# Optimization experiments

Measured on AMD Instinct MI355X. Metric: run time of the kernel, lower is better.

Reference implementation:

```python
import jax, jax.numpy as jnp
import numpy as np

B, C, H, W = 8, 256, 64, 64
CK = 64  # C // k with k=4


def setup_inputs() -> dict:
    key = jax.random.key(0)
    ks = jax.random.split(key, 5)
    s = 1.0 / np.sqrt(C)
    return {
        "x": jax.random.normal(ks[0], (B, C, H, W), dtype=jnp.float32),
        "wq": jax.random.normal(ks[1], (CK, C), dtype=jnp.float32) * s,
        "bq": jnp.zeros((CK,), dtype=jnp.float32),
        "wk": jax.random.normal(ks[2], (CK, C), dtype=jnp.float32) * s,
        "bk": jnp.zeros((CK,), dtype=jnp.float32),
        "wv": jax.random.normal(ks[3], (C, C), dtype=jnp.float32) * s,
        "bv": jnp.zeros((C,), dtype=jnp.float32),
        "wg": jax.random.normal(ks[4], (C, C), dtype=jnp.float32) * s,
        "bg": jnp.zeros((C,), dtype=jnp.float32),
    }


def reference(x, wq, bq, wk, bk, wv, bv, wg, bg):
    b, c, h, w = x.shape
    n = h * w
    xf = x.reshape(b, c, n)  # [B, C, N]
    # 1x1 convs are channel-wise matmuls
    q = jnp.einsum('oc,bcn->bon', wq, xf) + bq[None, :, None]  # [B, Ck, N]
    k = jnp.einsum('oc,bcn->bon', wk, xf) + bk[None, :, None]  # [B, Ck, N]
    v = jnp.einsum('oc,bcn->bon', wv, xf) + bv[None, :, None]  # [B, C, N]
    # energy[b,i,j] = q[b,:,i] . k[b,:,j]
    energy = jnp.einsum('bci,bcj->bij', q, k)  # [B, N, N]
    energy = jax.nn.elu(energy) / n
    out = jnp.einsum('bcn,bnj->bcj', v, energy).reshape(b, c, h, w)
    out = jnp.einsum('oc,bchw->bohw', wg, out) + bg[None, :, None, None]
    return out
```

## Files before the change

### kernel.cpp

```cpp
#include <hip/hip_runtime.h>
#include <math.h>

#define BATCH 8
#define CH    256
#define NPIX  4096
#define CKDIM 64

typedef __attribute__((ext_vector_type(8))) short short8;
typedef __attribute__((ext_vector_type(4))) float f32x4;

#define MFMA16x16(a, b, c) __builtin_amdgcn_mfma_f32_16x16x32_bf16((a), (b), (c), 0, 0, 0)

__device__ __forceinline__ unsigned short f2bf(float f) {
    union { float f; unsigned int u; } v; v.f = f;
    unsigned int u = v.u;
    u += 0x7fffu + ((u >> 16) & 1u);
    return (unsigned short)(u >> 16);
}

__global__ void prep_kernel(const float* __restrict__ wq, const float* __restrict__ bq,
                            const float* __restrict__ wk, const float* __restrict__ bk,
                            const float* __restrict__ wv, const float* __restrict__ bv,
                            const float* __restrict__ wg,
                            unsigned short* __restrict__ W_all, float* __restrict__ bias_all) {
    int o = blockIdx.x;
    int c = threadIdx.x;
    if (o < 64) {
        W_all[o * CH + c] = f2bf(wq[o * CH + c]);
        if (c == 0) bias_all[o] = bq[o];
    } else if (o < 128) {
        int oo = o - 64;
        W_all[o * CH + c] = f2bf(wk[oo * CH + c]);
        if (c == 0) bias_all[o] = bk[oo];
    } else {
        int oo = o - 128;
        float acc = 0.f;
        for (int m = 0; m < CH; ++m)
            acc += wg[oo * CH + m] * wv[m * CH + c];
        W_all[o * CH + c] = f2bf(acc);
        if (c == 0) {
            float b = 0.f;
            for (int m = 0; m < CH; ++m) b += wg[oo * CH + m] * bv[m];
            bias_all[o] = b;
        }
    }
}

__global__ void xpose_kernel(const float* __restrict__ x, unsigned short* __restrict__ xt) {
    __shared__ float Tl[64][65];
    int n0 = blockIdx.x * 64;
    int c0 = blockIdx.y * 64;
    int b  = blockIdx.z;
    int tid = threadIdx.x;

#pragma unroll
    for (int r = 0; r < 4; ++r) {
        int f  = r * 256 + tid;
        int c  = f >> 4;
        int n4 = f & 15;
        float4 v = *(const float4*)(x + ((size_t)b * CH + c0 + c) * NPIX + n0 + n4 * 4);
        Tl[n4 * 4 + 0][c] = v.x;
        Tl[n4 * 4 + 1][c] = v.y;
        Tl[n4 * 4 + 2][c] = v.z;
        Tl[n4 * 4 + 3][c] = v.w;
    }
    __syncthreads();
#pragma unroll
    for (int r = 0; r < 2; ++r) {
        int f    = r * 256 + tid;
        int nrow = f >> 3;
        int c8   = f & 7;
        unsigned int pk[4];
#pragma unroll
        for (int p = 0; p < 4; ++p) {
            unsigned int lo = f2bf(Tl[nrow][c8 * 8 + p * 2 + 0]);
            unsigned int hi = f2bf(Tl[nrow][c8 * 8 + p * 2 + 1]);
            pk[p] = lo | (hi << 16);
        }
        *(uint4*)(xt + ((size_t)b * NPIX + n0 + nrow) * CH + c0 + c8 * 8) = *(uint4*)pk;
    }
}

__global__ void qkv_mfma(const unsigned short* __restrict__ xt,
                         const unsigned short* __restrict__ W_all,
                         const float* __restrict__ bias_all,
                         unsigned short* __restrict__ qk, unsigned short* __restrict__ vp) {
    __shared__ __align__(16) unsigned short Xl[64][264];

    int n0   = blockIdx.x * 64;
    int b    = blockIdx.y;
    int tid  = threadIdx.x;
    int lane = tid & 63;
    int w    = tid >> 6;
    int col  = lane & 15;
    int quad = lane >> 4;

#pragma unroll
    for (int r = 0; r < 8; ++r) {
        int f   = r * 256 + tid;
        int row = f >> 5;
        int c8  = f & 31;
        *(uint4*)&Xl[row][c8 * 8] = *(const uint4*)(xt + ((size_t)b * NPIX + n0 + row) * CH + c8 * 8);
    }
    __syncthreads();

#pragma unroll
    for (int og = 0; og < 6; ++og) {
        int o0 = og * 64;
        const unsigned short* Arow = W_all + (size_t)(o0 + w * 16 + col) * CH + quad * 8;

        f32x4 acc[4];
#pragma unroll
        for (int t = 0; t < 4; ++t) acc[t] = (f32x4){0.f, 0.f, 0.f, 0.f};

#pragma unroll
        for (int kc = 0; kc < 8; ++kc) {
            short8 a = *(const short8*)(Arow + kc * 32);
#pragma unroll
            for (int nt = 0; nt < 4; ++nt) {
                short8 bb = *(const short8*)&Xl[nt * 16 + col][kc * 32 + quad * 8];
                acc[nt] = MFMA16x16(a, bb, acc[nt]);
            }
        }

        float4 bias = *(const float4*)(bias_all + o0 + w * 16 + quad * 4);
        float bs[4] = {bias.x, bias.y, bias.z, bias.w};

        if (og < 2) {
#pragma unroll
            for (int nt = 0; nt < 4; ++nt) {
                int n = n0 + nt * 16 + col;
                unsigned int pk[2];
#pragma unroll
                for (int p = 0; p < 2; ++p) {
                    unsigned int lo = f2bf(acc[nt][p * 2 + 0] + bs[p * 2 + 0]);
                    unsigned int hi = f2bf(acc[nt][p * 2 + 1] + bs[p * 2 + 1]);
                    pk[p] = lo | (hi << 16);
                }
                *(uint2*)(qk + ((size_t)b * NPIX + n) * 128 + o0 + w * 16 + quad * 4) = *(uint2*)pk;
            }
        } else {
#pragma unroll
            for (int nt = 0; nt < 4; ++nt) {
                int n = n0 + nt * 16 + col;
#pragma unroll
                for (int r = 0; r < 4; ++r) {
                    int oo = o0 - 128 + w * 16 + quad * 4 + r;
                    vp[((size_t)b * CH + oo) * NPIX + n] = f2bf(acc[nt][r] + bs[r]);
                }
            }
        }
    }
}

#define LPK 72
__global__ __launch_bounds__(512, 4)
void attn_v4(const unsigned short* __restrict__ qk,
             const unsigned short* __restrict__ vp,
             const float* __restrict__ bg, float* __restrict__ out) {
    __shared__ __align__(16) unsigned short Qt[64][LPK];
    __shared__ __align__(16) unsigned short Vl[256][LPK];
    __shared__ __align__(16) unsigned short St[64][LPK];

    int j0   = blockIdx.x * 64;
    int b    = blockIdx.y;
    int tid  = threadIdx.x;
    int lane = tid & 63;
    int w    = tid >> 6;
    int col  = lane & 15;
    int quad = lane >> 4;

    int tjA = w & 3;
    int tiP = (w >> 2) * 2;

    short8 bK[2];
#pragma unroll
    for (int ks = 0; ks < 2; ++ks)
        bK[ks] = *(const short8*)(qk + ((size_t)b * NPIX + j0 + tjA * 16 + col) * 128 + 64 + ks * 32 + quad * 8);

    f32x4 acc[2][4];
#pragma unroll
    for (int ot = 0; ot < 2; ++ot)
#pragma unroll
        for (int tj = 0; tj < 4; ++tj) acc[ot][tj] = (f32x4){0.f, 0.f, 0.f, 0.f};

    for (int i0 = 0; i0 < NPIX; i0 += 64) {
        __syncthreads();

        {
            int row = tid >> 3, q8 = tid & 7;
            *(uint4*)&Qt[row][q8 * 8] =
                *(const uint4*)(qk + ((size_t)b * NPIX + i0 + row) * 128 + q8 * 8);
        }
#pragma unroll
        for (int r = 0; r < 4; ++r) {
            int f = r * 512 + tid;
            int row = f >> 3, q8 = f & 7;
            *(uint4*)&Vl[row][q8 * 8] =
                *(const uint4*)(vp + ((size_t)b * CH + row) * NPIX + i0 + q8 * 8);
        }
        __syncthreads();

#pragma unroll
        for (int t = 0; t < 2; ++t) {
            int ti = tiP + t;
            short8 a0 = *(const short8*)&Qt[ti * 16 + col][quad * 8];
            short8 a1 = *(const short8*)&Qt[ti * 16 + col][32 + quad * 8];
            f32x4 s = (f32x4){0.f, 0.f, 0.f, 0.f};
            s = MFMA16x16(a0, bK[0], s);
            s = MFMA16x16(a1, bK[1], s);
            unsigned int pk[2];
#pragma unroll
            for (int p = 0; p < 2; ++p) {
                float e0 = s[p * 2 + 0];
                float e1 = s[p * 2 + 1];
                e0 = (e0 > 0.f) ? e0 : (__expf(e0) - 1.f);
                e1 = (e1 > 0.f) ? e1 : (__expf(e1) - 1.f);
                e0 *= (1.f / (float)NPIX);
                e1 *= (1.f / (float)NPIX);
                pk[p] = (unsigned int)f2bf(e0) | ((unsigned int)f2bf(e1) << 16);
            }
            *(uint2*)&St[tjA * 16 + col][ti * 16 + quad * 4] = *(uint2*)pk;
        }
        __syncthreads();

#pragma unroll
        for (int ks = 0; ks < 2; ++ks) {
            short8 sb[4];
#pragma unroll
            for (int tj = 0; tj < 4; ++tj)
                sb[tj] = *(const short8*)&St[tj * 16 + col][ks * 32 + quad * 8];
#pragma unroll
            for (int ot = 0; ot < 2; ++ot) {
                short8 bv = *(const short8*)&Vl[(w * 2 + ot) * 16 + col][ks * 32 + quad * 8];
#pragma unroll
                for (int tj = 0; tj < 4; ++tj)
                    acc[ot][tj] = MFMA16x16(sb[tj], bv, acc[ot][tj]);
            }
        }
    }

#pragma unroll
    for (int ot = 0; ot < 2; ++ot) {
        int o = (w * 2 + ot) * 16 + col;
        float bgv = bg[o];
#pragma unroll
        for (int tj = 0; tj < 4; ++tj) {
            int j = j0 + tj * 16 + quad * 4;
            float4 st;
            st.x = acc[ot][tj][0] + bgv;
            st.y = acc[ot][tj][1] + bgv;
            st.z = acc[ot][tj][2] + bgv;
            st.w = acc[ot][tj][3] + bgv;
            *(float4*)&out[((size_t)b * CH + o) * NPIX + j] = st;
        }
    }
}

extern "C" void kernel_launch(void* const* d_in, const int* in_sizes, int n_in,
                              void* d_out, int out_size, void* d_ws, size_t ws_size,
                              hipStream_t stream) {
    const float* x  = (const float*)d_in[0];
    const float* wq = (const float*)d_in[1];
    const float* bq = (const float*)d_in[2];
    const float* wk = (const float*)d_in[3];
    const float* bk = (const float*)d_in[4];
    const float* wv = (const float*)d_in[5];
    const float* bv = (const float*)d_in[6];
    const float* wg = (const float*)d_in[7];
    const float* bg = (const float*)d_in[8];
    float* out = (float*)d_out;

    unsigned short* W_all = (unsigned short*)d_ws;
    float* bias_all = (float*)(W_all + 384 * 256);
    unsigned short* xt = (unsigned short*)(bias_all + 384);
    unsigned short* qk = xt + (size_t)BATCH * NPIX * CH;
    unsigned short* vp = qk + (size_t)BATCH * NPIX * 128;

    prep_kernel<<<dim3(384), dim3(256), 0, stream>>>(wq, bq, wk, bk, wv, bv, wg, W_all, bias_all);
    xpose_kernel<<<dim3(NPIX / 64, CH / 64, BATCH), dim3(256), 0, stream>>>(x, xt);
    qkv_mfma<<<dim3(NPIX / 64, BATCH), dim3(256), 0, stream>>>(xt, W_all, bias_all, qk, vp);
    attn_v4<<<dim3(NPIX / 64, BATCH), dim3(512), 0, stream>>>(qk, vp, bg, out);
}
```

Measured before the change: 267.8 us.

## Software-pipeline attention loop with double-buffered Q/S and register-resident V

The attention kernel now double-buffers the Q tile and score tile in shared memory. Scores for tile t are computed while the V-multiply runs on the scores of tile t-1, which cuts the loop to a single barrier per iteration. V fragments are loaded straight from global memory into registers instead of being staged in shared memory. Q and K are split into separate contiguous buffers, and the weight-prep kernel is reorganized to compute 8 output rows per block with wg cached in shared memory. The changes raise register pressure and add prefetch complexity.

```diff
diff --git a/kernel.cpp b/kernel.cpp
--- a/kernel.cpp
+++ b/kernel.cpp
@@ -23,25 +23,41 @@
                             const float* __restrict__ wv, const float* __restrict__ bv,
                             const float* __restrict__ wg,
                             unsigned short* __restrict__ W_all, float* __restrict__ bias_all) {
-    int o = blockIdx.x;
-    int c = threadIdx.x;
-    if (o < 64) {
-        W_all[o * CH + c] = f2bf(wq[o * CH + c]);
-        if (c == 0) bias_all[o] = bq[o];
-    } else if (o < 128) {
-        int oo = o - 64;
-        W_all[o * CH + c] = f2bf(wk[oo * CH + c]);
-        if (c == 0) bias_all[o] = bk[oo];
+    int bo  = blockIdx.x;
+    int tid = threadIdx.x;
+    if (bo < 16) {
+        int r0 = bo * 8;
+#pragma unroll
+        for (int r = 0; r < 8; ++r) {
+            int o = r0 + r;
+            float v = (o < 64) ? wq[o * CH + tid] : wk[(o - 64) * CH + tid];
+            W_all[o * CH + tid] = f2bf(v);
+        }
+        if (tid < 8) {
+            int o = r0 + tid;
+            bias_all[o] = (o < 64) ? bq[o] : bk[o - 64];
+        }
     } else {
-        int oo = o - 128;
-        float acc = 0.f;
-        for (int m = 0; m < CH; ++m)
-            acc += wg[oo * CH + m] * wv[m * CH + c];
-        W_all[o * CH + c] = f2bf(acc);
-        if (c == 0) {
-            float b = 0.f;
-            for (int m = 0; m < CH; ++m) b += wg[oo * CH + m] * bv[m];
-            bias_all[o] = b;
+        int ob = (bo - 16) * 8;
+        __shared__ float wgl[8][256];
+#pragma unroll
+        for (int r = 0; r < 8; ++r) wgl[r][tid] = wg[(size_t)(ob + r) * CH + tid];
+        __syncthreads();
+        float acc[8];
+#pragma unroll
+        for (int r = 0; r < 8; ++r) acc[r] = 0.f;
+        for (int m = 0; m < CH; ++m) {
+            float wvv = wv[(size_t)m * CH + tid];
+#pragma unroll
+            for (int r = 0; r < 8; ++r) acc[r] += wgl[r][m] * wvv;
+        }
+#pragma unroll
+        for (int r = 0; r < 8; ++r)
+            W_all[(size_t)(128 + ob + r) * CH + tid] = f2bf(acc[r]);
+        if (tid < 8) {
+            float bb = 0.f;
+            for (int m = 0; m < CH; ++m) bb += wgl[tid][m] * bv[m];
+            bias_all[128 + ob + tid] = bb;
         }
     }
 }
@@ -84,7 +100,8 @@
 __global__ void qkv_mfma(const unsigned short* __restrict__ xt,
                          const unsigned short* __restrict__ W_all,
                          const float* __restrict__ bias_all,
-                         unsigned short* __restrict__ qk, unsigned short* __restrict__ vp) {
+                         unsigned short* __restrict__ qg, unsigned short* __restrict__ kg,
+                         unsigned short* __restrict__ vp) {
     __shared__ __align__(16) unsigned short Xl[64][264];
 
     int n0   = blockIdx.x * 64;
@@ -127,6 +144,7 @@
         float bs[4] = {bias.x, bias.y, bias.z, bias.w};
 
         if (og < 2) {
+            unsigned short* dst = (og == 0) ? qg : kg;
 #pragma unroll
             for (int nt = 0; nt < 4; ++nt) {
                 int n = n0 + nt * 16 + col;
@@ -137,7 +155,7 @@
                     unsigned int hi = f2bf(acc[nt][p * 2 + 1] + bs[p * 2 + 1]);
                     pk[p] = lo | (hi << 16);
                 }
-                *(uint2*)(qk + ((size_t)b * NPIX + n) * 128 + o0 + w * 16 + quad * 4) = *(uint2*)pk;
+                *(uint2*)(dst + ((size_t)b * NPIX + n) * 64 + w * 16 + quad * 4) = *(uint2*)pk;
             }
         } else {
 #pragma unroll
@@ -153,14 +171,14 @@
     }
 }
 
-#define LPK 72
+#define LQ 72
 __global__ __launch_bounds__(512, 4)
-void attn_v4(const unsigned short* __restrict__ qk,
+void attn_v6(const unsigned short* __restrict__ qg,
+             const unsigned short* __restrict__ kg,
              const unsigned short* __restrict__ vp,
              const float* __restrict__ bg, float* __restrict__ out) {
-    __shared__ __align__(16) unsigned short Qt[64][LPK];
-    __shared__ __align__(16) unsigned short Vl[256][LPK];
-    __shared__ __align__(16) unsigned short St[64][LPK];
+    __shared__ __align__(16) unsigned short Qt[2][64][LQ];
+    __shared__ __align__(16) unsigned short St[2][64][LQ];
 
     int j0   = blockIdx.x * 64;
     int b    = blockIdx.y;
@@ -170,13 +188,20 @@
     int col  = lane & 15;
     int quad = lane >> 4;
 
-    int tjA = w & 3;
-    int tiP = (w >> 2) * 2;
-
-    short8 bK[2];
-#pragma unroll
-    for (int ks = 0; ks < 2; ++ks)
-        bK[ks] = *(const short8*)(qk + ((size_t)b * NPIX + j0 + tjA * 16 + col) * 128 + 64 + ks * 32 + quad * 8);
+    int tiw = w >> 1;
+    int tjh = w & 1;
+
+    const size_t nb = (size_t)b * NPIX;
+    int srow = tid >> 3, sq8 = tid & 7;
+
+    short8 bK[2][2];
+#pragma unroll
+    for (int tjl = 0; tjl < 2; ++tjl)
+#pragma unroll
+        for (int ks = 0; ks < 2; ++ks)
+            bK[tjl][ks] = *(const short8*)(kg + (nb + j0 + (tjh * 2 + tjl) * 16 + col) * 64 + ks * 32 + quad * 8);
+
+    *(uint4*)&Qt[0][srow][sq8 * 8] = *(const uint4*)(qg + (nb + srow) * 64 + sq8 * 8);
 
     f32x4 acc[2][4];
 #pragma unroll
@@ -184,60 +209,96 @@
 #pragma unroll
         for (int tj = 0; tj < 4; ++tj) acc[ot][tj] = (f32x4){0.f, 0.f, 0.f, 0.f};
 
-    for (int i0 = 0; i0 < NPIX; i0 += 64) {
-        __syncthreads();
-
-        {
-            int row = tid >> 3, q8 = tid & 7;
-            *(uint4*)&Qt[row][q8 * 8] =
-                *(const uint4*)(qk + ((size_t)b * NPIX + i0 + row) * 128 + q8 * 8);
-        }
-#pragma unroll
-        for (int r = 0; r < 4; ++r) {
-            int f = r * 512 + tid;
-            int row = f >> 3, q8 = f & 7;
-            *(uint4*)&Vl[row][q8 * 8] =
-                *(const uint4*)(vp + ((size_t)b * CH + row) * NPIX + i0 + q8 * 8);
-        }
-        __syncthreads();
-
-#pragma unroll
-        for (int t = 0; t < 2; ++t) {
-            int ti = tiP + t;
-            short8 a0 = *(const short8*)&Qt[ti * 16 + col][quad * 8];
-            short8 a1 = *(const short8*)&Qt[ti * 16 + col][32 + quad * 8];
+    __syncthreads();
+
+    uint4 qn = *(const uint4*)(qg + (nb + 64 + srow) * 64 + sq8 * 8);
+    {
+        short8 aq0 = *(const short8*)&Qt[0][tiw * 16 + col][quad * 8];
+        short8 aq1 = *(const short8*)&Qt[0][tiw * 16 + col][32 + quad * 8];
+#pragma unroll
+        for (int tjl = 0; tjl < 2; ++tjl) {
             f32x4 s = (f32x4){0.f, 0.f, 0.f, 0.f};
-            s = MFMA16x16(a0, bK[0], s);
-            s = MFMA16x16(a1, bK[1], s);
+            s = MFMA16x16(aq0, bK[tjl][0], s);
+            s = MFMA16x16(aq1, bK[tjl][1], s);
             unsigned int pk[2];
 #pragma unroll
             for (int p = 0; p < 2; ++p) {
-                float e0 = s[p * 2 + 0];
-                float e1 = s[p * 2 + 1];
+                float e0 = s[p * 2 + 0], e1 = s[p * 2 + 1];
                 e0 = (e0 > 0.f) ? e0 : (__expf(e0) - 1.f);
                 e1 = (e1 > 0.f) ? e1 : (__expf(e1) - 1.f);
                 e0 *= (1.f / (float)NPIX);
                 e1 *= (1.f / (float)NPIX);
                 pk[p] = (unsigned int)f2bf(e0) | ((unsigned int)f2bf(e1) << 16);
             }
-            *(uint2*)&St[tjA * 16 + col][ti * 16 + quad * 4] = *(uint2*)pk;
-        }
-        __syncthreads();
+            *(uint2*)&St[0][(tjh * 2 + tjl) * 16 + col][tiw * 16 + quad * 4] = *(uint2*)pk;
+        }
+    }
+    *(uint4*)&Qt[1][srow][sq8 * 8] = qn;
+    uint4 aV[2][2];
+#pragma unroll
+    for (int ot = 0; ot < 2; ++ot)
+#pragma unroll
+        for (int ks = 0; ks < 2; ++ks)
+            aV[ot][ks] = *(const uint4*)(vp + ((size_t)b * CH + (2 * w + ot) * 16 + col) * NPIX + ks * 32 + quad * 8);
+    __syncthreads();
+
+    for (int t = 1; t < 64; ++t) {
+        int i0 = t * 64;
+        int p  = t & 1;
+        uint4 q2 = *(const uint4*)(qg + (nb + (((t + 1) & 63) * 64) + srow) * 64 + sq8 * 8);
+
+        short8 aq0 = *(const short8*)&Qt[p][tiw * 16 + col][quad * 8];
+        short8 aq1 = *(const short8*)&Qt[p][tiw * 16 + col][32 + quad * 8];
+#pragma unroll
+        for (int tjl = 0; tjl < 2; ++tjl) {
+            f32x4 s = (f32x4){0.f, 0.f, 0.f, 0.f};
+            s = MFMA16x16(aq0, bK[tjl][0], s);
+            s = MFMA16x16(aq1, bK[tjl][1], s);
+            unsigned int pk[2];
+#pragma unroll
+            for (int pp = 0; pp < 2; ++pp) {
+                float e0 = s[pp * 2 + 0], e1 = s[pp * 2 + 1];
+                e0 = (e0 > 0.f) ? e0 : (__expf(e0) - 1.f);
+                e1 = (e1 > 0.f) ? e1 : (__expf(e1) - 1.f);
+                e0 *= (1.f / (float)NPIX);
+                e1 *= (1.f / (float)NPIX);
+                pk[pp] = (unsigned int)f2bf(e0) | ((unsigned int)f2bf(e1) << 16);
+            }
+            *(uint2*)&St[p][(tjh * 2 + tjl) * 16 + col][tiw * 16 + quad * 4] = *(uint2*)pk;
+        }
+        *(uint4*)&Qt[p ^ 1][srow][sq8 * 8] = q2;
 
 #pragma unroll
         for (int ks = 0; ks < 2; ++ks) {
             short8 sb[4];
 #pragma unroll
             for (int tj = 0; tj < 4; ++tj)
-                sb[tj] = *(const short8*)&St[tj * 16 + col][ks * 32 + quad * 8];
-#pragma unroll
-            for (int ot = 0; ot < 2; ++ot) {
-                short8 bv = *(const short8*)&Vl[(w * 2 + ot) * 16 + col][ks * 32 + quad * 8];
+                sb[tj] = *(const short8*)&St[p ^ 1][tj * 16 + col][ks * 32 + quad * 8];
+#pragma unroll
+            for (int ot = 0; ot < 2; ++ot)
 #pragma unroll
                 for (int tj = 0; tj < 4; ++tj)
-                    acc[ot][tj] = MFMA16x16(sb[tj], bv, acc[ot][tj]);
-            }
-        }
+                    acc[ot][tj] = MFMA16x16(sb[tj], *(const short8*)&aV[ot][ks], acc[ot][tj]);
+        }
+#pragma unroll
+        for (int ot = 0; ot < 2; ++ot)
+#pragma unroll
+            for (int ks = 0; ks < 2; ++ks)
+                aV[ot][ks] = *(const uint4*)(vp + ((size_t)b * CH + (2 * w + ot) * 16 + col) * NPIX + i0 + ks * 32 + quad * 8);
+        __syncthreads();
+    }
+
+#pragma unroll
+    for (int ks = 0; ks < 2; ++ks) {
+        short8 sb[4];
+#pragma unroll
+        for (int tj = 0; tj < 4; ++tj)
+            sb[tj] = *(const short8*)&St[1][tj * 16 + col][ks * 32 + quad * 8];
+#pragma unroll
+        for (int ot = 0; ot < 2; ++ot)
+#pragma unroll
+            for (int tj = 0; tj < 4; ++tj)
+                acc[ot][tj] = MFMA16x16(sb[tj], *(const short8*)&aV[ot][ks], acc[ot][tj]);
     }
 
 #pragma unroll
@@ -274,11 +335,12 @@
     unsigned short* W_all = (unsigned short*)d_ws;
     float* bias_all = (float*)(W_all + 384 * 256);
     unsigned short* xt = (unsigned short*)(bias_all + 384);
-    unsigned short* qk = xt + (size_t)BATCH * NPIX * CH;
-    unsigned short* vp = qk + (size_t)BATCH * NPIX * 128;
-
-    prep_kernel<<<dim3(384), dim3(256), 0, stream>>>(wq, bq, wk, bk, wv, bv, wg, W_all, bias_all);
+    unsigned short* qg = xt + (size_t)BATCH * NPIX * CH;
+    unsigned short* kg = qg + (size_t)BATCH * NPIX * 64;
+    unsigned short* vp = kg + (size_t)BATCH * NPIX * 64;
+
+    prep_kernel<<<dim3(48), dim3(256), 0, stream>>>(wq, bq, wk, bk, wv, bv, wg, W_all, bias_all);
     xpose_kernel<<<dim3(NPIX / 64, CH / 64, BATCH), dim3(256), 0, stream>>>(x, xt);
-    qkv_mfma<<<dim3(NPIX / 64, BATCH), dim3(256), 0, stream>>>(xt, W_all, bias_all, qk, vp);
-    attn_v4<<<dim3(NPIX / 64, BATCH), dim3(512), 0, stream>>>(qk, vp, bg, out);
-}
+    qkv_mfma<<<dim3(NPIX / 64, BATCH), dim3(256), 0, stream>>>(xt, W_all, bias_all, qg, kg, vp);
+    attn_v6<<<dim3(NPIX / 64, BATCH), dim3(512), 0, stream>>>(qg, kg, vp, bg, out);
+}
```

New measurement: 274.9 us. 1.03x slower.
